# Kernel tuning notes

Measured on AMD Instinct MI355X. Metric: run time of the kernel, lower is better.

## Reference

```python
import jax, jax.numpy as jnp
import numpy as np

B, T, C, H = 8, 2048, 512, 512


def setup_inputs() -> dict:
    key = jax.random.key(0)
    ks = jax.random.split(key, 9)
    s = 1.0 / np.sqrt(C)
    return {
        "q": jax.random.normal(ks[0], (B, T, C), jnp.float32),
        "k": jax.random.normal(ks[1], (B, T, C), jnp.float32),
        "v": jax.random.normal(ks[2], (B, T, C), jnp.float32),
        "Wq": jax.random.normal(ks[3], (C, H), jnp.float32) * s,
        "bq": jax.random.normal(ks[4], (H,), jnp.float32) * 0.01,
        "Wk": jax.random.normal(ks[5], (C, H), jnp.float32) * s,
        "bk": jax.random.normal(ks[6], (H,), jnp.float32) * 0.01,
        "Wv": jax.random.normal(ks[7], (C, H), jnp.float32) * s,
        "bv": jax.random.normal(ks[8], (H,), jnp.float32) * 0.01,
    }


def reference(q, k, v, Wq, bq, Wk, bk, Wv, bv):
    # Linear projections (Real_Linear == nn.Linear): [B,T,C] @ [C,H] + [H]
    query = jnp.einsum('btc,ch->bth', q, Wq) + bq
    key_p = jnp.einsum('btc,ch->bth', k, Wk) + bk
    value = jnp.einsum('btc,ch->bth', v, Wv) + bv
    # energy = Q @ K^T / sqrt(H)  -> [B, T, T]
    energy = jnp.einsum('bth,byh->bty', query, key_p) / jnp.sqrt(jnp.asarray(H, query.dtype))
    attn = jax.nn.softmax(energy, axis=-1)
    # weighted value: [B, T, T] @ [B, T, H] -> [B, T, H]
    return jnp.einsum('bty,byh->bth', attn, value)
```

## Files before the change

kernel.cpp:

```cpp
#include <hip/hip_runtime.h>
#include <hip/hip_bf16.h>

typedef unsigned short u16;
typedef unsigned int u32;
typedef short s16x8 __attribute__((ext_vector_type(8)));
typedef float f32x4 __attribute__((ext_vector_type(4)));

#define NB 8
#define NT 2048
#define NC 512
#define NH 512

__device__ __forceinline__ u16 f2bf(float f) {
  unsigned u = __float_as_uint(f);
  u += 0x7FFFu + ((u >> 16) & 1u);
  return (u16)(u >> 16);
}

__device__ __forceinline__ void gld16(const u16* src, u16* lds_dst) {
  __builtin_amdgcn_global_load_lds(
      (const __attribute__((address_space(1))) u32*)src,
      (__attribute__((address_space(3))) u32*)lds_dst, 16, 0, 0);
}

__global__ __launch_bounds__(256) void wt_kernel(const float* __restrict__ W,
                                                 u16* __restrict__ WT) {
  __shared__ float tile[32][33];
  const int x = threadIdx.x & 31;
  const int y = threadIdx.x >> 5;
  const int k0 = blockIdx.x * 32, h0 = blockIdx.y * 32;
#pragma unroll
  for (int p = 0; p < 4; ++p)
    tile[y + 8 * p][x] = W[(size_t)(k0 + y + 8 * p) * NH + h0 + x];
  __syncthreads();
#pragma unroll
  for (int p = 0; p < 4; ++p)
    WT[(size_t)(h0 + y + 8 * p) * NC + k0 + x] = f2bf(tile[x][y + 8 * p]);
}

__global__ __launch_bounds__(256) void proj_kernel(const float* __restrict__ X,
                                                   const u16* __restrict__ WT,
                                                   const float* __restrict__ bias,
                                                   u16* __restrict__ Y) {
  __shared__ __align__(16) u16 Asub[128 * 40];
  __shared__ __align__(16) u16 Bsub[128 * 40];
  const int t = threadIdx.x;
  const int lane = t & 63;
  const int w = t >> 6;
  const int l16 = lane & 15;
  const int ko8 = (lane >> 4) * 8;
  const int m0 = blockIdx.y * 128;
  const int n0 = blockIdx.x * 128;
  const int wr = (w >> 1) * 64, wc = (w & 1) * 64;
  f32x4 acc[4][4] = {};

  for (int kt = 0; kt < 16; ++kt) {
    const int k0 = kt * 32;
#pragma unroll
    for (int p = 0; p < 4; ++p) {
      int c = t + 256 * p;
      int r = c >> 3, cc = (c & 7) * 4;
      const float4 v = *(const float4*)&X[(size_t)(m0 + r) * NC + k0 + cc];
      ushort4 bb;
      bb.x = f2bf(v.x); bb.y = f2bf(v.y); bb.z = f2bf(v.z); bb.w = f2bf(v.w);
      *(ushort4*)&Asub[r * 40 + cc] = bb;
    }
#pragma unroll
    for (int p = 0; p < 2; ++p) {
      int c = t + 256 * p;
      int r = c >> 2, cc = (c & 3) * 8;
      *(int4*)&Bsub[r * 40 + cc] = *(const int4*)&WT[(size_t)(n0 + r) * NC + k0 + cc];
    }
    __syncthreads();
    s16x8 af[4], bf[4];
#pragma unroll
    for (int i = 0; i < 4; ++i)
      af[i] = *(const s16x8*)&Asub[(wr + i * 16 + l16) * 40 + ko8];
#pragma unroll
    for (int j = 0; j < 4; ++j)
      bf[j] = *(const s16x8*)&Bsub[(wc + j * 16 + l16) * 40 + ko8];
#pragma unroll
    for (int i = 0; i < 4; ++i)
#pragma unroll
      for (int j = 0; j < 4; ++j)
        acc[i][j] = __builtin_amdgcn_mfma_f32_16x16x32_bf16(af[i], bf[j], acc[i][j], 0, 0, 0);
    __syncthreads();
  }
  const int rg = (lane >> 4) * 4;
#pragma unroll
  for (int i = 0; i < 4; ++i)
#pragma unroll
    for (int j = 0; j < 4; ++j) {
      const int col = n0 + wc + j * 16 + l16;
      const float bcol = bias[col];
#pragma unroll
      for (int jj = 0; jj < 4; ++jj) {
        const int row = m0 + wr + i * 16 + rg + jj;
        Y[(size_t)row * NH + col] = f2bf(acc[i][j][jj] + bcol);
      }
    }
}

__global__ __launch_bounds__(256) void vt_kernel(const u16* __restrict__ Vp,
                                                 u16* __restrict__ VpT) {
  __shared__ u16 tile[32][33];
  const int x = threadIdx.x & 31;
  const int y = threadIdx.x >> 5;
  const int t0 = blockIdx.x * 32, h0 = blockIdx.y * 32, b = blockIdx.z;
  const u16* src = Vp + (size_t)b * NT * NH;
  u16* dst = VpT + (size_t)b * NH * NT;
#pragma unroll
  for (int p = 0; p < 4; ++p)
    tile[y + 8 * p][x] = src[(size_t)(t0 + y + 8 * p) * NH + h0 + x];
  __syncthreads();
#pragma unroll
  for (int p = 0; p < 4; ++p)
    dst[(size_t)(h0 + y + 8 * p) * NT + t0 + x] = tile[x][y + 8 * p];
}

__global__ __launch_bounds__(512, 2) void flash_partial(const u16* __restrict__ Qp,
                                                        const u16* __restrict__ Kp,
                                                        const u16* __restrict__ VpT,
                                                        float* __restrict__ O0,
                                                        float* __restrict__ O1,
                                                        float* __restrict__ mlws) {
  __shared__ __align__(16) u16 Klds[2][32 * 512];
  __shared__ __align__(16) u16 Vlds[2][32 * 512];

  const int t = threadIdx.x;
  const int lane = t & 63;
  const int w = t >> 6;
  const int l16 = lane & 15;
  const int g = lane >> 4;
  const int g8 = g * 8;
  const int b = blockIdx.x;
  const int q0 = blockIdx.y * 128;
  const int z = blockIdx.z;
  const int qg = q0 + w * 16 + l16;
  const float kscale = 0.044194173824159216f;

  s16x8 qf[16];
  {
    const u16* qrow = Qp + (size_t)(b * NT + qg) * NH;
#pragma unroll
    for (int ks = 0; ks < 16; ++ks)
      qf[ks] = *(const s16x8*)&qrow[ks * 32 + g8];
  }

  f32x4 oacc[32] = {};
  float m_run = -1e30f, l_run = 0.f;

  const u16* kbat = Kp + (size_t)(b * NT + z * 1024) * NH;
  const u16* vbat = VpT + (size_t)b * NH * NT + z * 1024;

#define STAGE(buf, it)                                                         \
  {                                                                            \
    _Pragma("unroll")                                                          \
    for (int r = 0; r < 4; ++r) {                                              \
      const int i = w * 4 + r;                                      \
             \
      gld16(kbat + (size_t)((it) * 32 + ((i & 1) << 4) + l16) * NH             \
                 + ((i >> 1) << 5) + g8,                                       \
            &Klds[buf][i * 512]);                                              \
                                 \
      gld16(vbat + (size_t)(i * 16 + l16) * NT + (it) * 32 + g8,               \
            &Vlds[buf][i * 512]);                                              \
    }                                                                          \
  }

  STAGE(0, 0)
  __syncthreads();

  int pb = 0;
  for (int it = 0; it < 32; ++it) {
    if (it < 31) STAGE(pb ^ 1, it + 1)
    f32x4 s0 = {}, s1 = {};
#pragma unroll
    for (int ks = 0; ks < 16; ++ks) {
      s16x8 kf0 = *(const s16x8*)&Klds[pb][(ks * 2 + 0) * 512 + lane * 8];
      s16x8 kf1 = *(const s16x8*)&Klds[pb][(ks * 2 + 1) * 512 + lane * 8];
      s0 = __builtin_amdgcn_mfma_f32_16x16x32_bf16(kf0, qf[ks], s0, 0, 0, 0);
      s1 = __builtin_amdgcn_mfma_f32_16x16x32_bf16(kf1, qf[ks], s1, 0, 0, 0);
    }
    float pv[8];
#pragma unroll
    for (int j = 0; j < 4; ++j) { pv[j] = s0[j] * kscale; pv[4 + j] = s1[j] * kscale; }
    float mx = pv[0];
#pragma unroll
    for (int j = 1; j < 8; ++j) mx = fmaxf(mx, pv[j]);
    mx = fmaxf(mx, __shfl_xor(mx, 16, 64));
    mx = fmaxf(mx, __shfl_xor(mx, 32, 64));
    if (__any(mx > m_run)) {
      const float m_new = fmaxf(m_run, mx);
      const float scale = __expf(m_run - m_new);
#pragma unroll
      for (int ht = 0; ht < 32; ++ht) {
        oacc[ht][0] *= scale; oacc[ht][1] *= scale;
        oacc[ht][2] *= scale; oacc[ht][3] *= scale;
      }
      l_run *= scale;
      m_run = m_new;
    }
    float ts = 0.f;
#pragma unroll
    for (int j = 0; j < 8; ++j) { pv[j] = __expf(pv[j] - m_run); ts += pv[j]; }
    ts += __shfl_xor(ts, 16, 64);
    ts += __shfl_xor(ts, 32, 64);
    l_run += ts;
    u32 b0 = ((u32)f2bf(pv[1]) << 16) | f2bf(pv[0]);
    u32 b1 = ((u32)f2bf(pv[3]) << 16) | f2bf(pv[2]);
    u32 b2 = ((u32)f2bf(pv[5]) << 16) | f2bf(pv[4]);
    u32 b3 = ((u32)f2bf(pv[7]) << 16) | f2bf(pv[6]);
    const int srcA = (g & 1) * 32 + l16;
    const int srcB = srcA + 16;
    u32 x0 = (u32)__shfl((int)b0, srcA, 64);
    u32 x1 = (u32)__shfl((int)b1, srcA, 64);
    u32 x2 = (u32)__shfl((int)b2, srcA, 64);
    u32 x3 = (u32)__shfl((int)b3, srcA, 64);
    u32 y0 = (u32)__shfl((int)b0, srcB, 64);
    u32 y1 = (u32)__shfl((int)b1, srcB, 64);
    u32 y2 = (u32)__shfl((int)b2, srcB, 64);
    u32 y3 = (u32)__shfl((int)b3, srcB, 64);
    const bool hi = (lane >> 5) & 1;
    union { u32 u[4]; s16x8 v; } pf;
    pf.u[0] = hi ? x2 : x0;
    pf.u[1] = hi ? x3 : x1;
    pf.u[2] = hi ? y2 : y0;
    pf.u[3] = hi ? y3 : y1;
#pragma unroll
    for (int ht = 0; ht < 32; ++ht) {
      s16x8 vf = *(const s16x8*)&Vlds[pb][ht * 512 + lane * 8];
      oacc[ht] = __builtin_amdgcn_mfma_f32_16x16x32_bf16(vf, pf.v, oacc[ht], 0, 0, 0);
    }
    __syncthreads();
    pb ^= 1;
  }
  float* obase = (z ? O1 : O0) + (size_t)(b * NT + qg) * NH;
#pragma unroll
  for (int ht = 0; ht < 32; ++ht) {
    float4 st;
    st.x = oacc[ht][0]; st.y = oacc[ht][1];
    st.z = oacc[ht][2]; st.w = oacc[ht][3];
    *(float4*)&obase[ht * 16 + g * 4] = st;
  }
  if (g == 0) {
    const size_t row = (size_t)b * NT + qg;
    mlws[row * 4 + z * 2 + 0] = m_run;
    mlws[row * 4 + z * 2 + 1] = l_run;
  }
#undef STAGE
}

__global__ __launch_bounds__(128) void merge_kernel(float* __restrict__ out,
                                                    const float* __restrict__ O1,
                                                    const float* __restrict__ mlws) {
  const size_t row = blockIdx.x;
  const float m0 = mlws[row * 4 + 0], l0 = mlws[row * 4 + 1];
  const float m1 = mlws[row * 4 + 2], l1 = mlws[row * 4 + 3];
  const float m = fmaxf(m0, m1);
  const float a0 = __expf(m0 - m), a1 = __expf(m1 - m);
  const float inv = 1.f / (a0 * l0 + a1 * l1);
  const float c0 = a0 * inv, c1 = a1 * inv;
  const size_t idx = row * NH + threadIdx.x * 4;
  float4 o0 = *(const float4*)&out[idx];
  float4 o1 = *(const float4*)&O1[idx];
  float4 r;
  r.x = c0 * o0.x + c1 * o1.x;
  r.y = c0 * o0.y + c1 * o1.y;
  r.z = c0 * o0.z + c1 * o1.z;
  r.w = c0 * o0.w + c1 * o1.w;
  *(float4*)&out[idx] = r;
}

__global__ __launch_bounds__(256, 1) void flash_kernel(const u16* __restrict__ Qp,
                                                       const u16* __restrict__ Kp,
                                                       const u16* __restrict__ VpT,
                                                       float* __restrict__ out) {
  __shared__ __align__(16) u16 Klds[2][32 * 512];
  __shared__ __align__(16) u16 Vlds[2][32 * 512];

  const int t = threadIdx.x;
  const int lane = t & 63;
  const int w = t >> 6;
  const int l16 = lane & 15;
  const int g = lane >> 4;
  const int g8 = g * 8;
  const int b = blockIdx.x;
  const int q0 = blockIdx.y * 64;
  const int qg = q0 + w * 16 + l16;
  const float kscale = 0.044194173824159216f;

  s16x8 qf[16];
  {
    const u16* qrow = Qp + (size_t)(b * NT + qg) * NH;
#pragma unroll
    for (int ks = 0; ks < 16; ++ks)
      qf[ks] = *(const s16x8*)&qrow[ks * 32 + g8];
  }
  f32x4 oacc[32] = {};
  float m_run = -1e30f, l_run = 0.f;
  const u16* kbat = Kp + (size_t)b * NT * NH;
  const u16* vbat = VpT + (size_t)b * NH * NT;

#pragma unroll
  for (int r = 0; r < 8; ++r) {
    const int i = w * 8 + r;
    gld16(kbat + (size_t)(((i & 1) << 4) + l16) * NH + ((i >> 1) << 5) + g8,
          &Klds[0][i * 512]);
    gld16(vbat + (size_t)(i * 16 + l16) * NT + g8, &Vlds[0][i * 512]);
  }
  __syncthreads();

  int pb = 0;
  for (int it = 0; it < 64; ++it) {
    if (it < 63) {
      const int kv1 = (it + 1) * 32;
      const int nb = pb ^ 1;
#pragma unroll
      for (int r = 0; r < 8; ++r) {
        const int i = w * 8 + r;
        gld16(kbat + (size_t)(kv1 + ((i & 1) << 4) + l16) * NH + ((i >> 1) << 5) + g8,
              &Klds[nb][i * 512]);
        gld16(vbat + (size_t)(i * 16 + l16) * NT + kv1 + g8, &Vlds[nb][i * 512]);
      }
    }
    f32x4 s0 = {}, s1 = {};
#pragma unroll
    for (int ks = 0; ks < 16; ++ks) {
      s16x8 kf0 = *(const s16x8*)&Klds[pb][(ks * 2 + 0) * 512 + lane * 8];
      s16x8 kf1 = *(const s16x8*)&Klds[pb][(ks * 2 + 1) * 512 + lane * 8];
      s0 = __builtin_amdgcn_mfma_f32_16x16x32_bf16(kf0, qf[ks], s0, 0, 0, 0);
      s1 = __builtin_amdgcn_mfma_f32_16x16x32_bf16(kf1, qf[ks], s1, 0, 0, 0);
    }
    float pv[8];
#pragma unroll
    for (int j = 0; j < 4; ++j) { pv[j] = s0[j] * kscale; pv[4 + j] = s1[j] * kscale; }
    float mx = pv[0];
#pragma unroll
    for (int j = 1; j < 8; ++j) mx = fmaxf(mx, pv[j]);
    mx = fmaxf(mx, __shfl_xor(mx, 16, 64));
    mx = fmaxf(mx, __shfl_xor(mx, 32, 64));
    if (__any(mx > m_run)) {
      const float m_new = fmaxf(m_run, mx);
      const float scale = __expf(m_run - m_new);
#pragma unroll
      for (int ht = 0; ht < 32; ++ht) {
        oacc[ht][0] *= scale; oacc[ht][1] *= scale;
        oacc[ht][2] *= scale; oacc[ht][3] *= scale;
      }
      l_run *= scale;
      m_run = m_new;
    }
    float ts = 0.f;
#pragma unroll
    for (int j = 0; j < 8; ++j) { pv[j] = __expf(pv[j] - m_run); ts += pv[j]; }
    ts += __shfl_xor(ts, 16, 64);
    ts += __shfl_xor(ts, 32, 64);
    l_run += ts;
    u32 b0 = ((u32)f2bf(pv[1]) << 16) | f2bf(pv[0]);
    u32 b1 = ((u32)f2bf(pv[3]) << 16) | f2bf(pv[2]);
    u32 b2 = ((u32)f2bf(pv[5]) << 16) | f2bf(pv[4]);
    u32 b3 = ((u32)f2bf(pv[7]) << 16) | f2bf(pv[6]);
    const int srcA = (g & 1) * 32 + l16;
    const int srcB = srcA + 16;
    u32 x0 = (u32)__shfl((int)b0, srcA, 64);
    u32 x1 = (u32)__shfl((int)b1, srcA, 64);
    u32 x2 = (u32)__shfl((int)b2, srcA, 64);
    u32 x3 = (u32)__shfl((int)b3, srcA, 64);
    u32 y0 = (u32)__shfl((int)b0, srcB, 64);
    u32 y1 = (u32)__shfl((int)b1, srcB, 64);
    u32 y2 = (u32)__shfl((int)b2, srcB, 64);
    u32 y3 = (u32)__shfl((int)b3, srcB, 64);
    const bool hi = (lane >> 5) & 1;
    union { u32 u[4]; s16x8 v; } pf;
    pf.u[0] = hi ? x2 : x0;
    pf.u[1] = hi ? x3 : x1;
    pf.u[2] = hi ? y2 : y0;
    pf.u[3] = hi ? y3 : y1;
#pragma unroll
    for (int ht = 0; ht < 32; ++ht) {
      s16x8 vf = *(const s16x8*)&Vlds[pb][ht * 512 + lane * 8];
      oacc[ht] = __builtin_amdgcn_mfma_f32_16x16x32_bf16(vf, pf.v, oacc[ht], 0, 0, 0);
    }
    __syncthreads();
    pb ^= 1;
  }
  const float inv = 1.f / l_run;
  float* obase = out + (size_t)(b * NT + qg) * NH;
#pragma unroll
  for (int ht = 0; ht < 32; ++ht) {
    float4 st;
    st.x = oacc[ht][0] * inv; st.y = oacc[ht][1] * inv;
    st.z = oacc[ht][2] * inv; st.w = oacc[ht][3] * inv;
    *(float4*)&obase[ht * 16 + g * 4] = st;
  }
}

extern "C" void kernel_launch(void* const* d_in, const int* in_sizes, int n_in,
                              void* d_out, int out_size, void* d_ws, size_t ws_size,
                              hipStream_t stream) {
  (void)in_sizes; (void)n_in; (void)out_size;
  const float* q  = (const float*)d_in[0];
  const float* k  = (const float*)d_in[1];
  const float* v  = (const float*)d_in[2];
  const float* Wq = (const float*)d_in[3];
  const float* bq = (const float*)d_in[4];
  const float* Wk = (const float*)d_in[5];
  const float* bk = (const float*)d_in[6];
  const float* Wv = (const float*)d_in[7];
  const float* bv = (const float*)d_in[8];
  float* out = (float*)d_out;

  u16* ws   = (u16*)d_ws;
  u16* WqT  = ws;
  u16* WkT  = WqT + (size_t)NC * NH;
  u16* WvT  = WkT + (size_t)NC * NH;
  u16* Qp   = WvT + (size_t)NC * NH;
  u16* Kp   = Qp + (size_t)NB * NT * NH;
  u16* Vp   = Kp + (size_t)NB * NT * NH;
  u16* VpT  = Vp + (size_t)NB * NT * NH;
  u16* endb = VpT + (size_t)NB * NT * NH;
  float* O1   = (float*)endb;
  float* mlws = O1 + (size_t)NB * NT * NH;
  const size_t need = (size_t)((char*)(mlws + (size_t)NB * NT * 4) - (char*)d_ws);

  wt_kernel<<<dim3(16, 16), 256, 0, stream>>>(Wq, WqT);
  wt_kernel<<<dim3(16, 16), 256, 0, stream>>>(Wk, WkT);
  wt_kernel<<<dim3(16, 16), 256, 0, stream>>>(Wv, WvT);

  proj_kernel<<<dim3(4, 128), 256, 0, stream>>>(q, WqT, bq, Qp);
  proj_kernel<<<dim3(4, 128), 256, 0, stream>>>(k, WkT, bk, Kp);
  proj_kernel<<<dim3(4, 128), 256, 0, stream>>>(v, WvT, bv, Vp);

  vt_kernel<<<dim3(64, 16, NB), 256, 0, stream>>>(Vp, VpT);

  if (ws_size >= need) {
    flash_partial<<<dim3(NB, NT / 128, 2), 512, 0, stream>>>(Qp, Kp, VpT, out, O1, mlws);
    merge_kernel<<<dim3(NB * NT), 128, 0, stream>>>(out, O1, mlws);
  } else {
    flash_kernel<<<dim3(NB, NT / 64), 256, 0, stream>>>(Qp, Kp, VpT, out);
  }
}
```

Measured before the change: 234.4 us.

## Double-buffer projection GEMM, raise MFMA priority, use lazy softmax rescale

The projection GEMM now prefetches the next K-tile of X and W into registers while MFMAs run on the current LDS buffer, then writes it into a second LDS buffer, so global-load latency overlaps compute. The attention kernel wraps both MFMA loops in s_setprio to favor matrix issue across waves. It also rescales the online softmax only when the running max grows by more than 8, skipping most rescales of the 32 accumulators. The costs are doubled LDS and more registers in the projection, and the lazy rescale lets exponentials reach up to e^8 before renormalizing, which is fine in fp32 but changes rounding slightly.

```diff
diff --git a/kernel.cpp b/kernel.cpp
--- a/kernel.cpp
+++ b/kernel.cpp
@@ -42,8 +42,8 @@
                                                    const u16* __restrict__ WT,
                                                    const float* __restrict__ bias,
                                                    u16* __restrict__ Y) {
-  __shared__ __align__(16) u16 Asub[128 * 40];
-  __shared__ __align__(16) u16 Bsub[128 * 40];
+  __shared__ __align__(16) u16 Asub[2][128 * 40];
+  __shared__ __align__(16) u16 Bsub[2][128 * 40];
   const int t = threadIdx.x;
   const int lane = t & 63;
   const int w = t >> 6;
@@ -54,38 +54,64 @@
   const int wr = (w >> 1) * 64, wc = (w & 1) * 64;
   f32x4 acc[4][4] = {};
 
+  float4 areg[4];
+  int4 breg[2];
+#define PLOAD(kt)                                                              \
+  {                                                                            \
+    const int k0_ = (kt) * 32;                                                 \
+    _Pragma("unroll")                                                          \
+    for (int p = 0; p < 4; ++p) {                                              \
+      int c = t + 256 * p;                                                     \
+      areg[p] = *(const float4*)&X[(size_t)(m0 + (c >> 3)) * NC + k0_ + (c & 7) * 4]; \
+    }                                                                          \
+    _Pragma("unroll")                                                          \
+    for (int p = 0; p < 2; ++p) {                                              \
+      int c = t + 256 * p;                                                     \
+      breg[p] = *(const int4*)&WT[(size_t)(n0 + (c >> 2)) * NC + k0_ + (c & 3) * 8];  \
+    }                                                                          \
+  }
+#define PWRITE(buf)                                                            \
+  {                                                                            \
+    _Pragma("unroll")                                                          \
+    for (int p = 0; p < 4; ++p) {                                              \
+      int c = t + 256 * p;                                                     \
+      ushort4 bb;                                                              \
+      bb.x = f2bf(areg[p].x); bb.y = f2bf(areg[p].y);                          \
+      bb.z = f2bf(areg[p].z); bb.w = f2bf(areg[p].w);                          \
+      *(ushort4*)&Asub[buf][(c >> 3) * 40 + (c & 7) * 4] = bb;                 \
+    }                                                                          \
+    _Pragma("unroll")                                                          \
+    for (int p = 0; p < 2; ++p) {                                              \
+      int c = t + 256 * p;                                                     \
+      *(int4*)&Bsub[buf][(c >> 2) * 40 + (c & 3) * 8] = breg[p];               \
+    }                                                                          \
+  }
+
+  PLOAD(0)
+  PWRITE(0)
+  __syncthreads();
+
+  int pb = 0;
   for (int kt = 0; kt < 16; ++kt) {
-    const int k0 = kt * 32;
-#pragma unroll
-    for (int p = 0; p < 4; ++p) {
-      int c = t + 256 * p;
-      int r = c >> 3, cc = (c & 7) * 4;
-      const float4 v = *(const float4*)&X[(size_t)(m0 + r) * NC + k0 + cc];
-      ushort4 bb;
-      bb.x = f2bf(v.x); bb.y = f2bf(v.y); bb.z = f2bf(v.z); bb.w = f2bf(v.w);
-      *(ushort4*)&Asub[r * 40 + cc] = bb;
-    }
-#pragma unroll
-    for (int p = 0; p < 2; ++p) {
-      int c = t + 256 * p;
-      int r = c >> 2, cc = (c & 3) * 8;
-      *(int4*)&Bsub[r * 40 + cc] = *(const int4*)&WT[(size_t)(n0 + r) * NC + k0 + cc];
-    }
-    __syncthreads();
+    if (kt < 15) PLOAD(kt + 1)
     s16x8 af[4], bf[4];
 #pragma unroll
     for (int i = 0; i < 4; ++i)
-      af[i] = *(const s16x8*)&Asub[(wr + i * 16 + l16) * 40 + ko8];
+      af[i] = *(const s16x8*)&Asub[pb][(wr + i * 16 + l16) * 40 + ko8];
 #pragma unroll
     for (int j = 0; j < 4; ++j)
-      bf[j] = *(const s16x8*)&Bsub[(wc + j * 16 + l16) * 40 + ko8];
+      bf[j] = *(const s16x8*)&Bsub[pb][(wc + j * 16 + l16) * 40 + ko8];
 #pragma unroll
     for (int i = 0; i < 4; ++i)
 #pragma unroll
       for (int j = 0; j < 4; ++j)
         acc[i][j] = __builtin_amdgcn_mfma_f32_16x16x32_bf16(af[i], bf[j], acc[i][j], 0, 0, 0);
+    if (kt < 15) PWRITE(pb ^ 1)
     __syncthreads();
-  }
+    pb ^= 1;
+  }
+#undef PLOAD
+#undef PWRITE
   const int rg = (lane >> 4) * 4;
 #pragma unroll
   for (int i = 0; i < 4; ++i)
@@ -158,11 +184,9 @@
     _Pragma("unroll")                                                          \
     for (int r = 0; r < 4; ++r) {                                              \
       const int i = w * 4 + r;                                      \
-             \
       gld16(kbat + (size_t)((it) * 32 + ((i & 1) << 4) + l16) * NH             \
                  + ((i >> 1) << 5) + g8,                                       \
             &Klds[buf][i * 512]);                                              \
-                                 \
       gld16(vbat + (size_t)(i * 16 + l16) * NT + (it) * 32 + g8,               \
             &Vlds[buf][i * 512]);                                              \
     }                                                                          \
@@ -175,6 +199,7 @@
   for (int it = 0; it < 32; ++it) {
     if (it < 31) STAGE(pb ^ 1, it + 1)
     f32x4 s0 = {}, s1 = {};
+    __builtin_amdgcn_s_setprio(1);
 #pragma unroll
     for (int ks = 0; ks < 16; ++ks) {
       s16x8 kf0 = *(const s16x8*)&Klds[pb][(ks * 2 + 0) * 512 + lane * 8];
@@ -182,6 +207,7 @@
       s0 = __builtin_amdgcn_mfma_f32_16x16x32_bf16(kf0, qf[ks], s0, 0, 0, 0);
       s1 = __builtin_amdgcn_mfma_f32_16x16x32_bf16(kf1, qf[ks], s1, 0, 0, 0);
     }
+    __builtin_amdgcn_s_setprio(0);
     float pv[8];
 #pragma unroll
     for (int j = 0; j < 4; ++j) { pv[j] = s0[j] * kscale; pv[4 + j] = s1[j] * kscale; }
@@ -190,7 +216,7 @@
     for (int j = 1; j < 8; ++j) mx = fmaxf(mx, pv[j]);
     mx = fmaxf(mx, __shfl_xor(mx, 16, 64));
     mx = fmaxf(mx, __shfl_xor(mx, 32, 64));
-    if (__any(mx > m_run)) {
+    if (__any(mx > m_run + 8.f)) {
       const float m_new = fmaxf(m_run, mx);
       const float scale = __expf(m_run - m_new);
 #pragma unroll
@@ -227,11 +253,13 @@
     pf.u[1] = hi ? x3 : x1;
     pf.u[2] = hi ? y2 : y0;
     pf.u[3] = hi ? y3 : y1;
+    __builtin_amdgcn_s_setprio(1);
 #pragma unroll
     for (int ht = 0; ht < 32; ++ht) {
       s16x8 vf = *(const s16x8*)&Vlds[pb][ht * 512 + lane * 8];
       oacc[ht] = __builtin_amdgcn_mfma_f32_16x16x32_bf16(vf, pf.v, oacc[ht], 0, 0, 0);
     }
+    __builtin_amdgcn_s_setprio(0);
     __syncthreads();
     pb ^= 1;
   }
```

Measured after the change: 228.6 us. -2.5%, faster.
